# Kernel optimization log

Hardware: AMD Instinct MI355X
Metric: run time of the kernel (lower is better)

Reference implementation:

```python
import jax, jax.numpy as jnp
import numpy as np

N = 20000      # num clique nodes
E = 320000     # num edges
H = 256        # hidden_channels
OUT = 128      # out_channels
T = 3          # num_timesteps
NEG = 0.01     # GAT negative_slope
NA = 60000     # num atoms (unused arg sizing)


def setup_inputs() -> dict:
    key = jax.random.key(0)
    ks = jax.random.split(key, 12)
    s = 1.0 / np.sqrt(H)
    return {
        "x_clique": jax.random.normal(ks[0], (N, H), jnp.float32),
        "W_gat": jax.random.normal(ks[1], (H, H), jnp.float32) * s,
        "att_src": jax.random.normal(ks[2], (H,), jnp.float32) * s,
        "att_dst": jax.random.normal(ks[3], (H,), jnp.float32) * s,
        "gat_bias": jnp.zeros((H,), jnp.float32),
        "W_ih": jax.random.normal(ks[4], (3 * H, H), jnp.float32) * s,
        "W_hh": jax.random.normal(ks[5], (3 * H, H), jnp.float32) * s,
        "b_ih": jnp.zeros((3 * H,), jnp.float32),
        "b_hh": jnp.zeros((3 * H,), jnp.float32),
        "lin_W": jax.random.normal(ks[6], (OUT, H), jnp.float32) * s,
        "lin_b": jnp.zeros((OUT,), jnp.float32),
        "atom2clique_index": jax.random.randint(ks[7], (2, NA), 0, N, jnp.int64),
        "mol_batch": jax.random.randint(ks[8], (NA,), 0, 32, jnp.int64),
        "clique_batch": jax.random.randint(ks[9], (N,), 0, 32, jnp.int64),
        "clique_edge_index": jax.random.randint(ks[10], (2, E), 0, N, jnp.int64),
    }


def _gat_conv(h, W_gat, att_src, att_dst, gat_bias, src, dst):
    # PyG GATConv, heads=1, no self loops. h: [N,H]
    xp = h @ W_gat.T                                   # [N,H]
    a_e = jax.nn.leaky_relu((xp @ att_src)[src] + (xp @ att_dst)[dst], NEG)  # [E]
    # segment softmax over destination nodes
    m = jax.ops.segment_max(a_e, dst, num_segments=N)  # [N] (-inf for empty)
    e = jnp.exp(a_e - m[dst])                          # [E]
    denom = jax.ops.segment_sum(e, dst, num_segments=N)
    coef = e / jnp.maximum(denom[dst], 1e-16)          # [E]
    out = jax.ops.segment_sum(coef[:, None] * xp[src], dst, num_segments=N)
    return out + gat_bias


def _gru_cell(x, h, W_ih, W_hh, b_ih, b_hh):
    gx = x @ W_ih.T + b_ih                             # [N,3H]
    gh = h @ W_hh.T + b_hh                             # [N,3H]
    xr, xz, xn = jnp.split(gx, 3, axis=-1)
    hr, hz, hn = jnp.split(gh, 3, axis=-1)
    r = jax.nn.sigmoid(xr + hr)
    z = jax.nn.sigmoid(xz + hz)
    n = jnp.tanh(xn + r * hn)
    return (1.0 - z) * n + z * h


def reference(x_clique, W_gat, att_src, att_dst, gat_bias, W_ih, W_hh, b_ih, b_hh,
              lin_W, lin_b, atom2clique_index, mol_batch, clique_batch,
              clique_edge_index):
    src = clique_edge_index[0]
    dst = clique_edge_index[1]
    h = x_clique
    for _ in range(T):  # fixed, small timestep count
        m = _gat_conv(h, W_gat, att_src, att_dst, gat_bias, src, dst)
        m = jax.nn.elu(m)  # dropout p=0.0 -> identity
        h = _gru_cell(m, h, W_ih, W_hh, b_ih, b_hh)
    return h @ lin_W.T + lin_b  # [N, OUT]
```

## Files before the change

### kernel.cpp

```cpp
#include <hip/hip_runtime.h>
#include <math.h>

#define NNODES 20000
#define NROWP  20096
#define NEDGES 320000
#define HDIM   256
#define ODIM   128
#define TSTEPS 3
#define KCAT   512

typedef __bf16 bf16x8 __attribute__((ext_vector_type(8)));
typedef __bf16 bf16x4 __attribute__((ext_vector_type(4)));
typedef float  f32x4  __attribute__((ext_vector_type(4)));

#define LOG2E 1.44269504f
__device__ __forceinline__ float fexp2_(float x){ return __builtin_amdgcn_exp2f(x); }
__device__ __forceinline__ float frcp_(float x){ return __builtin_amdgcn_rcpf(x); }
__device__ __forceinline__ float fsig_(float x){ return frcp_(1.f + fexp2_(-LOG2E*x)); }
__device__ __forceinline__ float ftanh_(float x){ float t = fexp2_(2.f*LOG2E*x); return 1.f - 2.f*frcp_(t+1.f); }
__device__ __forceinline__ float felu_(float x){ return (x>0.f)? x : (fexp2_(LOG2E*x)-1.f); }

__device__ __forceinline__ void load_lds16(const void* g, void* l){
  __builtin_amdgcn_global_load_lds((const __attribute__((address_space(1))) void*)g,
                                   (__attribute__((address_space(3))) void*)l, 16, 0, 0);
}

__device__ __forceinline__ bf16x8 lds_frag64(const __bf16* Ls, int rowbase, int lane, int kk){
  int row = rowbase + (lane&15);
  int g = (lane>>4) + (kk<<2);
  int slot = (row<<3) + (g ^ (row&7));
  return *(const bf16x8*)&Ls[slot<<3];
}

template<int NWG>
__device__ __forceinline__ int xcd_swz(int b){
  constexpr int Q = NWG/8, R = NWG%8;
  int x = b & 7, i = b >> 3;
  if (R == 0) return x*Q + i;
  return (x < R) ? (x*(Q+1) + i) : (R*(Q+1) + (x-R)*Q + i);
}

#define WAIT_VM(n) asm volatile("s_waitcnt vmcnt(" #n ")" ::: "memory")
#define WAIT_LGKM0 asm volatile("s_waitcnt lgkmcnt(0)" ::: "memory")


__global__ void setup1_kernel(const int* __restrict__ dst, int* __restrict__ deg,
                              const float* __restrict__ xc, __bf16* __restrict__ Acat,
                              const float* __restrict__ Wih, const float* __restrict__ Whh,
                              const float* __restrict__ Wg, const float* __restrict__ Lw,
                              __bf16* __restrict__ Bf, __bf16* __restrict__ wgb,
                              __bf16* __restrict__ lwb, float* __restrict__ asad){
  int i = blockIdx.x*blockDim.x + threadIdx.x;
  if (i < NEDGES) atomicAdd(&deg[dst[i]], 1);
  if (i < NNODES*64){
    int row = i>>6, c = (i&63)<<2;
    float4 v = *(const float4*)&xc[(size_t)row*HDIM + c];
    bf16x4 o; o[0]=(__bf16)v.x; o[1]=(__bf16)v.y; o[2]=(__bf16)v.z; o[3]=(__bf16)v.w;
    *(bf16x4*)&Acat[(size_t)row*KCAT + 256 + c] = o;
  }
  if (i < 1024*128){
    int row = i>>7, kc = (i&127)<<2;
    int gate = row>>8, c = row&255;
    float4 v = make_float4(0,0,0,0);
    if (gate==0 || gate==1){
      v = (kc<256) ? *(const float4*)&Wih[(size_t)(gate*256+c)*HDIM + kc]
                   : *(const float4*)&Whh[(size_t)(gate*256+c)*HDIM + kc-256];
    } else if (gate==2){
      if (kc<256) v = *(const float4*)&Wih[(size_t)(512+c)*HDIM + kc];
    } else {
      if (kc>=256) v = *(const float4*)&Whh[(size_t)(512+c)*HDIM + kc-256];
    }
    bf16x4 o; o[0]=(__bf16)v.x; o[1]=(__bf16)v.y; o[2]=(__bf16)v.z; o[3]=(__bf16)v.w;
    *(bf16x4*)&Bf[(size_t)row*KCAT + kc] = o;
  } else if (i < 1024*128 + 256*64){
    int j = i - 1024*128;
    float4 v = ((const float4*)Wg)[j];
    bf16x4 o; o[0]=(__bf16)v.x; o[1]=(__bf16)v.y; o[2]=(__bf16)v.z; o[3]=(__bf16)v.w;
    ((bf16x4*)wgb)[j] = o;
  } else if (i < 1024*128 + 256*64 + 128*64){
    int j = i - 1024*128 - 256*64;
    float4 v = ((const float4*)Lw)[j];
    bf16x4 o; o[0]=(__bf16)v.x; o[1]=(__bf16)v.y; o[2]=(__bf16)v.z; o[3]=(__bf16)v.w;
    ((bf16x4*)lwb)[j] = o;
  }
  if (i < 2*NNODES) asad[i] = 0.f;
}

__global__ void scan_kernel(const int* __restrict__ deg, int* __restrict__ rowptr){
  const int PER = 20;
  int tid = threadIdx.x, lane = tid&63, w = tid>>6;
  int base = tid*PER;
  int v[PER]; int s = 0;
  #pragma unroll
  for (int k=0;k<PER;k++){
    v[k] = (base+k < NNODES)? deg[base+k] : 0;
    s += v[k];
  }
  int incl = s;
  #pragma unroll
  for (int off=1; off<64; off<<=1){
    int t = __shfl_up(incl, off);
    if (lane >= off) incl += t;
  }
  __shared__ int wtot[16];
  if (lane==63) wtot[w] = incl;
  __syncthreads();
  if (w==0 && lane<16){
    int x = wtot[lane];
    #pragma unroll
    for (int off=1; off<16; off<<=1){
      int t = __shfl_up(x, off);
      if (lane >= off) x += t;
    }
    wtot[lane] = x;
  }
  __syncthreads();
  int wbase = (w>0)? wtot[w-1] : 0;
  int run = wbase + incl - s;
  #pragma unroll
  for (int k=0;k<PER;k++){
    if (base+k < NNODES) rowptr[base+k] = run;
    run += v[k];
  }
  if (tid==1023) rowptr[NNODES] = wbase + incl;
}

__global__ void scatter_kernel(const int* __restrict__ src, const int* __restrict__ dst,
                               const int* __restrict__ rowptr, int* __restrict__ fill,
                               int* __restrict__ ssrc){
  int e = blockIdx.x*blockDim.x + threadIdx.x;
  if (e < NEDGES){
    int d = dst[e];
    int pos = rowptr[d] + atomicAdd(&fill[d], 1);
    ssrc[pos] = src[e];
  }
}

template<int YC, bool F32OUT, bool ALPHA, int NWG>
__global__ __launch_bounds__(256,3)
void mfma_gemm_sm(const __bf16* __restrict__ A, int lda,
                  const __bf16* __restrict__ B,
                  const float* __restrict__ bias,
                  __bf16* __restrict__ Cb, float* __restrict__ Cf,
                  int ldc, int Mreal,
                  const float* __restrict__ att_s, const float* __restrict__ att_d,
                  float* __restrict__ as_, float* __restrict__ ad_){
  __shared__ __bf16 As[2][64*64];
  __shared__ __bf16 Bs[2][128*64];
  int wgid = xcd_swz<NWG>(blockIdx.x);
  int r0 = (wgid/YC)*64, c0 = (wgid%YC)*128;
  int tx = threadIdx.x, lane = tx&63, w = tx>>6;
  int rbase = (w&1)*32, cbase = (w>>1)*64;
  f32x4 acc[2][4] = {};

  auto stage = [&](int k0, int s){
    #pragma unroll
    for (int q=0;q<2;q++){
      int idx = q*256 + w*64 + lane;
      int row = idx>>3, kg = (idx&7) ^ (row&7);
      load_lds16(A + (size_t)(r0+row)*lda + k0 + (kg<<3),
                 (char*)&As[s][0] + (q*256 + w*64)*16);
    }
    #pragma unroll
    for (int q=0;q<4;q++){
      int idx = q*256 + w*64 + lane;
      int row = idx>>3, kg = (idx&7) ^ (row&7);
      load_lds16(B + (size_t)(c0+row)*HDIM + k0 + (kg<<3),
                 (char*)&Bs[s][0] + (q*256 + w*64)*16);
    }
  };

  stage(0, 0);
  stage(64, 1);
  #pragma unroll
  for (int t=0; t<HDIM/64; t++){
    const int cur = t & 1;
    if (t == HDIM/64-1) { WAIT_VM(0); } else { WAIT_VM(6); }
    __builtin_amdgcn_s_barrier();
    #pragma unroll
    for (int kk=0;kk<2;kk++){
      bf16x8 a[2], bb[4];
      #pragma unroll
      for (int i=0;i<2;i++) a[i] = lds_frag64(&As[cur][0], rbase + i*16, lane, kk);
      #pragma unroll
      for (int j=0;j<4;j++) bb[j] = lds_frag64(&Bs[cur][0], cbase + j*16, lane, kk);
      #pragma unroll
      for (int i=0;i<2;i++)
        #pragma unroll
        for (int j=0;j<4;j++)
          acc[i][j] = __builtin_amdgcn_mfma_f32_16x16x32_bf16(a[i], bb[j], acc[i][j], 0,0,0);
    }
    WAIT_LGKM0;
    __builtin_amdgcn_s_barrier();
    if (t+2 < HDIM/64) stage((t+2)*64, cur);
  }
  int grb = r0 + rbase, gcb = c0 + cbase;
  #pragma unroll
  for (int i=0;i<2;i++){
    #pragma unroll
    for (int j=0;j<4;j++){
      int gc = gcb + j*16 + (lane&15);
      float bv = F32OUT ? bias[gc] : 0.f;
      #pragma unroll
      for (int r=0;r<4;r++){
        int gr = grb + i*16 + ((lane>>4)<<2) + r;
        if (gr >= Mreal) continue;
        float v = acc[i][j][r] + bv;
        if (F32OUT) Cf[(size_t)gr*ldc + gc] = v;
        else        Cb[(size_t)gr*ldc + gc] = (__bf16)v;
      }
    }
  }
  if (ALPHA){
    float ps[2][4] = {}, pd[2][4] = {};
    #pragma unroll
    for (int j=0;j<4;j++){
      int gc = gcb + j*16 + (lane&15);
      float sv = att_s[gc], dv = att_d[gc];
      #pragma unroll
      for (int i=0;i<2;i++)
        #pragma unroll
        for (int r=0;r<4;r++){
          ps[i][r] += acc[i][j][r]*sv;
          pd[i][r] += acc[i][j][r]*dv;
        }
    }
    #pragma unroll
    for (int m=1;m<16;m<<=1){
      #pragma unroll
      for (int i=0;i<2;i++)
        #pragma unroll
        for (int r=0;r<4;r++){
          ps[i][r] += __shfl_xor(ps[i][r], m);
          pd[i][r] += __shfl_xor(pd[i][r], m);
        }
    }
    if ((lane&15)==0){
      #pragma unroll
      for (int i=0;i<2;i++)
        #pragma unroll
        for (int r=0;r<4;r++){
          int gr = grb + i*16 + ((lane>>4)<<2) + r;
          if (gr < Mreal){
            atomicAdd(&as_[gr], ps[i][r]);
            atomicAdd(&ad_[gr], pd[i][r]);
          }
        }
    }
  }
}

__global__ __launch_bounds__(256,4)
void gat_aggregate_kernel(const __bf16* __restrict__ xpb, const float* __restrict__ as_,
                          const float* __restrict__ ad_, const int* __restrict__ rowptr,
                          const int* __restrict__ ssrc, const float* __restrict__ gat_bias,
                          __bf16* __restrict__ Acat){
  int node = blockIdx.x*4 + (threadIdx.x>>6);
  int lane = threadIdx.x & 63;
  if (node >= NNODES) return;
  int beg = rowptr[node], end = rowptr[node+1];
  int deg = end - beg;
  float adv = ad_[node];
  int half = lane>>5, col = lane&31;

  float acc[8] = {0,0,0,0,0,0,0,0};

  if (deg <= 64){
    float a = -INFINITY; int sreg = 0;
    if (lane < deg){
      sreg = ssrc[beg+lane];
      a = as_[sreg] + adv;
      a = (a>0.f)? a : 0.01f*a;
    }
    float mx = a;
    #pragma unroll
    for (int off=32; off; off>>=1) mx = fmaxf(mx, __shfl_xor(mx,off));
    float e = (lane<deg)? fexp2_(LOG2E*(a-mx)) : 0.f;
    float sm = e;
    #pragma unroll
    for (int off=32; off; off>>=1) sm += __shfl_xor(sm,off);
    float creg = e*frcp_(fmaxf(sm,1e-16f));

    int j = 0;
    for (; j+16<=deg; j+=16){
      float cc[8]; int rr[8]; bf16x8 vv[8];
      #pragma unroll
      for (int k=0;k<8;k++){
        cc[k] = __shfl(creg, j+2*k+half);
        rr[k] = __shfl(sreg, j+2*k+half);
      }
      #pragma unroll
      for (int k=0;k<8;k++) vv[k] = *(const bf16x8*)&xpb[(size_t)rr[k]*HDIM + col*8];
      #pragma unroll
      for (int k=0;k<8;k++)
        #pragma unroll
        for (int t=0;t<8;t++) acc[t] += cc[k]*(float)vv[k][t];
    }
    for (; j+8<=deg; j+=8){
      float cc[4]; int rr[4]; bf16x8 vv[4];
      #pragma unroll
      for (int k=0;k<4;k++){
        cc[k] = __shfl(creg, j+2*k+half);
        rr[k] = __shfl(sreg, j+2*k+half);
      }
      #pragma unroll
      for (int k=0;k<4;k++) vv[k] = *(const bf16x8*)&xpb[(size_t)rr[k]*HDIM + col*8];
      #pragma unroll
      for (int k=0;k<4;k++)
        #pragma unroll
        for (int t=0;t<8;t++) acc[t] += cc[k]*(float)vv[k][t];
    }
    for (; j+4<=deg; j+=4){
      float c0=__shfl(creg,j+half),  c1=__shfl(creg,j+2+half);
      int   r0=__shfl(sreg,j+half),  r1=__shfl(sreg,j+2+half);
      bf16x8 v0 = *(const bf16x8*)&xpb[(size_t)r0*HDIM + col*8];
      bf16x8 v1 = *(const bf16x8*)&xpb[(size_t)r1*HDIM + col*8];
      #pragma unroll
      for (int t=0;t<8;t++) acc[t] += c0*(float)v0[t] + c1*(float)v1[t];
    }
    for (; j<deg; j+=2){
      int jj = j + half;
      float cf = __shfl(creg, jj);
      int   rw = __shfl(sreg, jj);
      if (jj < deg){
        bf16x8 v = *(const bf16x8*)&xpb[(size_t)rw*HDIM + col*8];
        #pragma unroll
        for (int t=0;t<8;t++) acc[t] += cf*(float)v[t];
      }
    }
  } else {
    float mx = -INFINITY;
    for (int e=beg+lane; e<end; e+=64){
      float a = as_[ssrc[e]] + adv;
      a = (a>0.f)? a : 0.01f*a;
      mx = fmaxf(mx, a);
    }
    #pragma unroll
    for (int off=32; off; off>>=1) mx = fmaxf(mx, __shfl_xor(mx,off));
    float sm = 0.f;
    for (int e=beg+lane; e<end; e+=64){
      float a = as_[ssrc[e]] + adv;
      a = (a>0.f)? a : 0.01f*a;
      sm += fexp2_(LOG2E*(a-mx));
    }
    #pragma unroll
    for (int off=32; off; off>>=1) sm += __shfl_xor(sm,off);
    float rsc = frcp_(fmaxf(sm,1e-16f));
    for (int j=0; j<deg; j+=2){
      int jj = j + half;
      if (jj < deg){
        int rw = ssrc[beg+jj];
        float a = as_[rw] + adv;
        a = (a>0.f)? a : 0.01f*a;
        float cf = fexp2_(LOG2E*(a-mx))*rsc;
        bf16x8 v = *(const bf16x8*)&xpb[(size_t)rw*HDIM + col*8];
        #pragma unroll
        for (int t=0;t<8;t++) acc[t] += cf*(float)v[t];
      }
    }
  }

  #pragma unroll
  for (int t=0;t<8;t++) acc[t] += __shfl_down(acc[t], 32);
  if (half==0){
    float4 b0 = *(const float4*)&gat_bias[col*8];
    float4 b1 = *(const float4*)&gat_bias[col*8+4];
    float bb[8] = {b0.x,b0.y,b0.z,b0.w,b1.x,b1.y,b1.z,b1.w};
    bf16x8 ov;
    #pragma unroll
    for (int t=0;t<8;t++) ov[t] = (__bf16)felu_(acc[t]+bb[t]);
    *(bf16x8*)&Acat[(size_t)node*KCAT + col*8] = ov;
  }
}

#define RB128 (NROWP/128)
__global__ __launch_bounds__(256,4)
void gru_mfma_kernel(const __bf16* __restrict__ Acat, __bf16* __restrict__ AcatN,
                     const __bf16* __restrict__ Bf,
                     const float* __restrict__ bih, const float* __restrict__ bhh,
                     float* __restrict__ as_, float* __restrict__ ad_){
  __shared__ __bf16 As[128*64];
  __shared__ __bf16 Bs[96*64];
  int wgid = xcd_swz<RB128*8>(blockIdx.x);
  int r0 = (wgid>>3)*128, c0 = (wgid&7)*32;
  int tx = threadIdx.x, lane = tx&63, w = tx>>6;
  int rbase = w*32;
  f32x4 acc[4][2][2] = {};

  auto stage = [&](int k0, int tg){
    #pragma unroll
    for (int q=0;q<4;q++){
      int idx = q*256 + w*64 + lane;
      int row = idx>>3, kg = (idx&7) ^ (row&7);
      load_lds16(Acat + (size_t)(r0+row)*KCAT + k0 + (kg<<3),
                 (char*)As + (q*256 + w*64)*16);
    }
    #pragma unroll
    for (int q=0;q<3;q++){
      int idx = q*256 + w*64 + lane;
      int row = idx>>3, kg = (idx&7) ^ (row&7);
      int gsel = row>>5;
      int grow = (gsel==2 ? tg : gsel)*256 + c0 + (row&31);
      load_lds16(Bf + (size_t)grow*KCAT + k0 + (kg<<3),
                 (char*)Bs + (q*256 + w*64)*16);
    }
  };

  #pragma unroll
  for (int t=0; t<KCAT/64; t++){
    stage(t*64, (t<4)?2:3);
    __syncthreads();
    #pragma unroll
    for (int kk=0;kk<2;kk++){
      bf16x8 a[2], b0[2], b1[2], bt[2];
      #pragma unroll
      for (int i=0;i<2;i++) a[i] = lds_frag64(As, rbase + i*16, lane, kk);
      #pragma unroll
      for (int j=0;j<2;j++){
        b0[j] = lds_frag64(Bs, 0  + j*16, lane, kk);
        b1[j] = lds_frag64(Bs, 32 + j*16, lane, kk);
        bt[j] = lds_frag64(Bs, 64 + j*16, lane, kk);
      }
      #pragma unroll
      for (int i=0;i<2;i++)
        #pragma unroll
        for (int j=0;j<2;j++){
          acc[0][i][j] = __builtin_amdgcn_mfma_f32_16x16x32_bf16(a[i], b0[j], acc[0][i][j], 0,0,0);
          acc[1][i][j] = __builtin_amdgcn_mfma_f32_16x16x32_bf16(a[i], b1[j], acc[1][i][j], 0,0,0);
          if (t < 4)
            acc[2][i][j] = __builtin_amdgcn_mfma_f32_16x16x32_bf16(a[i], bt[j], acc[2][i][j], 0,0,0);
          else
            acc[3][i][j] = __builtin_amdgcn_mfma_f32_16x16x32_bf16(a[i], bt[j], acc[3][i][j], 0,0,0);
        }
    }
    __syncthreads();
  }
  int grb = r0 + rbase;
  #pragma unroll
  for (int i=0;i<2;i++){
    #pragma unroll
    for (int j=0;j<2;j++){
      int gc = c0 + j*16 + (lane&15);
      float br_ = bih[gc]     + bhh[gc];
      float bz_ = bih[256+gc] + bhh[256+gc];
      float bnx = bih[512+gc];
      float bnh = bhh[512+gc];
      #pragma unroll
      for (int r=0;r<4;r++){
        int gr = grb + i*16 + ((lane>>4)<<2) + r;
        if (gr >= NNODES) continue;
        float hold = (float)Acat[(size_t)gr*KCAT + 256 + gc];
        float rr = fsig_(acc[0][i][j][r] + br_);
        float zz = fsig_(acc[1][i][j][r] + bz_);
        float nn = ftanh_(acc[2][i][j][r] + bnx + rr*(acc[3][i][j][r] + bnh));
        AcatN[(size_t)gr*KCAT + 256 + gc] = (__bf16)((1.f-zz)*nn + zz*hold);
      }
    }
  }
  if ((wgid&7)==0 && (lane&15)==0){
    #pragma unroll
    for (int i=0;i<2;i++)
      #pragma unroll
      for (int r=0;r<4;r++){
        int gr = grb + i*16 + ((lane>>4)<<2) + r;
        if (gr < NNODES){ as_[gr] = 0.f; ad_[gr] = 0.f; }
      }
  }
}

extern "C" void kernel_launch(void* const* d_in, const int* in_sizes, int n_in,
                              void* d_out, int out_size, void* d_ws, size_t ws_size,
                              hipStream_t stream) {
  const float* x_clique = (const float*)d_in[0];
  const float* W_gat    = (const float*)d_in[1];
  const float* att_src  = (const float*)d_in[2];
  const float* att_dst  = (const float*)d_in[3];
  const float* gat_bias = (const float*)d_in[4];
  const float* W_ih     = (const float*)d_in[5];
  const float* W_hh     = (const float*)d_in[6];
  const float* b_ih     = (const float*)d_in[7];
  const float* b_hh     = (const float*)d_in[8];
  const float* lin_W    = (const float*)d_in[9];
  const float* lin_b    = (const float*)d_in[10];
  const int*   eidx     = (const int*)d_in[14];
  float* out = (float*)d_out;

  const int* src = eidx;
  const int* dst = eidx + NEDGES;

  const size_t ACAT = (size_t)NROWP*KCAT;
  __bf16* AcA  = (__bf16*)d_ws;
  __bf16* AcB  = AcA + ACAT;
  __bf16* xpb  = AcB + ACAT;
  __bf16* Bf   = xpb + (size_t)NROWP*HDIM;
  __bf16* wgb  = Bf  + (size_t)1024*KCAT;
  __bf16* lwb  = wgb + (size_t)HDIM*HDIM;
  float* as_   = (float*)(lwb + (size_t)ODIM*HDIM);
  float* ad_   = as_ + NNODES;
  int* deg     = (int*)(ad_ + NNODES);
  int* fill    = deg + NNODES;
  int* rowptr  = fill + NNODES;
  int* ssrc    = rowptr + (NNODES+1);

  hipMemsetAsync(deg, 0, 2*NNODES*sizeof(int), stream);
  setup1_kernel<<<NNODES*64/256, 256, 0, stream>>>(
      dst, deg, x_clique, AcA, W_ih, W_hh, W_gat, lin_W, Bf, wgb, lwb, as_);
  scan_kernel<<<1, 1024, 0, stream>>>(deg, rowptr);
  scatter_kernel<<<(NEDGES+255)/256, 256, 0, stream>>>(src, dst, rowptr, fill, ssrc);

  const int RB64 = NROWP/64;
  __bf16* Ac = AcA;
  __bf16* An = AcB;
  for (int t=0; t<TSTEPS; t++){
    mfma_gemm_sm<2,false,true,(NROWP/64)*2><<<RB64*2, 256, 0, stream>>>(
        Ac + 256, KCAT, wgb, nullptr, xpb, nullptr, HDIM, NNODES,
        att_src, att_dst, as_, ad_);
    gat_aggregate_kernel<<<(NNODES+3)/4, 256, 0, stream>>>(xpb, as_, ad_, rowptr, ssrc, gat_bias, Ac);
    gru_mfma_kernel<<<RB128*8, 256, 0, stream>>>(Ac, An, Bf, b_ih, b_hh, as_, ad_);
    __bf16* tmp = Ac; Ac = An; An = tmp;
  }
  mfma_gemm_sm<1,true,false,NROWP/64><<<RB64, 256, 0, stream>>>(
      Ac + 256, KCAT, lwb, lin_b, nullptr, out, ODIM, NNODES,
      nullptr, nullptr, nullptr, nullptr);
}
```

Before: 336.6 us.

## Fuse CSR build into setup and first GEMM launches, dropping memset/scan/scatter kernels

The degree histogram and prefix scan move into one extra 1024-thread block of the setup kernel, using packed 16-bit counters in LDS, so the memset and the separate scan kernel go away. The scatter of source indices becomes extra blocks appended to the first timestep's GAT projection GEMM launch. Those blocks use a copied rowptr as an atomic cursor, so the separate fill array is no longer needed. This cuts three launches and one memset. The cost is that a single block now serially processes all 320k edges for the histogram, which could sit on the critical path.

Measured after the change: 354.6 us. 1.05x slower.

```diff
diff --git a/kernel.cpp b/kernel.cpp
--- a/kernel.cpp
+++ b/kernel.cpp
@@ -8,6 +8,9 @@
 #define ODIM   128
 #define TSTEPS 3
 #define KCAT   512
+#define RB64   (NROWP/64)
+#define RB128  (NROWP/128)
+#define SCAT_NB ((NEDGES+255)/256)
 
 typedef __bf16 bf16x8 __attribute__((ext_vector_type(8)));
 typedef __bf16 bf16x4 __attribute__((ext_vector_type(4)));
@@ -44,14 +47,70 @@
 #define WAIT_LGKM0 asm volatile("s_waitcnt lgkmcnt(0)" ::: "memory")
 
 
-__global__ void setup1_kernel(const int* __restrict__ dst, int* __restrict__ deg,
-                              const float* __restrict__ xc, __bf16* __restrict__ Acat,
-                              const float* __restrict__ Wih, const float* __restrict__ Whh,
-                              const float* __restrict__ Wg, const float* __restrict__ Lw,
-                              __bf16* __restrict__ Bf, __bf16* __restrict__ wgb,
-                              __bf16* __restrict__ lwb, float* __restrict__ asad){
-  int i = blockIdx.x*blockDim.x + threadIdx.x;
-  if (i < NEDGES) atomicAdd(&deg[dst[i]], 1);
+__global__ __launch_bounds__(1024)
+void setup_fat(const int* __restrict__ src, const int* __restrict__ dst,
+               const float* __restrict__ xc, __bf16* __restrict__ Acat,
+               const float* __restrict__ Wih, const float* __restrict__ Whh,
+               const float* __restrict__ Wg, const float* __restrict__ Lw,
+               __bf16* __restrict__ Bf, __bf16* __restrict__ wgb,
+               __bf16* __restrict__ lwb, float* __restrict__ asad,
+               int* __restrict__ rowptr, int* __restrict__ rowptr2){
+  __shared__ int ldeg[NNODES/2];
+  __shared__ int wtot[16];
+  int tx = threadIdx.x;
+
+  if (blockIdx.x == 1250){
+    for (int k=tx; k<NNODES/2; k+=1024) ldeg[k] = 0;
+    __syncthreads();
+    for (int e=tx*4; e<NEDGES; e+=4096){
+      int4 d4 = *(const int4*)&dst[e];
+      atomicAdd(&ldeg[d4.x>>1], 1 << ((d4.x&1)<<4));
+      atomicAdd(&ldeg[d4.y>>1], 1 << ((d4.y&1)<<4));
+      atomicAdd(&ldeg[d4.z>>1], 1 << ((d4.z&1)<<4));
+      atomicAdd(&ldeg[d4.w>>1], 1 << ((d4.w&1)<<4));
+    }
+    __syncthreads();
+    const int PER = 20;
+    int lane = tx&63, w = tx>>6;
+    int base = tx*PER;
+    int v[PER]; int s = 0;
+    #pragma unroll
+    for (int k=0;k<PER;k++){
+      int n = base+k;
+      v[k] = (n < NNODES)? ((ldeg[n>>1] >> ((n&1)<<4)) & 0xffff) : 0;
+      s += v[k];
+    }
+    int incl = s;
+    #pragma unroll
+    for (int off=1; off<64; off<<=1){
+      int t = __shfl_up(incl, off);
+      if (lane >= off) incl += t;
+    }
+    if (lane==63) wtot[w] = incl;
+    __syncthreads();
+    if (w==0 && lane<16){
+      int x = wtot[lane];
+      #pragma unroll
+      for (int off=1; off<16; off<<=1){
+        int t = __shfl_up(x, off);
+        if (lane >= off) x += t;
+      }
+      wtot[lane] = x;
+    }
+    __syncthreads();
+    int wbase = (w>0)? wtot[w-1] : 0;
+    int run = wbase + incl - s;
+    #pragma unroll
+    for (int k=0;k<PER;k++){
+      int n = base+k;
+      if (n < NNODES){ rowptr[n] = run; rowptr2[n] = run; }
+      run += v[k];
+    }
+    if (tx==1023) rowptr[NNODES] = wbase + incl;
+    return;
+  }
+
+  int i = blockIdx.x*1024 + tx;
   if (i < NNODES*64){
     int row = i>>6, c = (i&63)<<2;
     float4 v = *(const float4*)&xc[(size_t)row*HDIM + c];
@@ -86,57 +145,7 @@
   if (i < 2*NNODES) asad[i] = 0.f;
 }
 
-__global__ void scan_kernel(const int* __restrict__ deg, int* __restrict__ rowptr){
-  const int PER = 20;
-  int tid = threadIdx.x, lane = tid&63, w = tid>>6;
-  int base = tid*PER;
-  int v[PER]; int s = 0;
-  #pragma unroll
-  for (int k=0;k<PER;k++){
-    v[k] = (base+k < NNODES)? deg[base+k] : 0;
-    s += v[k];
-  }
-  int incl = s;
-  #pragma unroll
-  for (int off=1; off<64; off<<=1){
-    int t = __shfl_up(incl, off);
-    if (lane >= off) incl += t;
-  }
-  __shared__ int wtot[16];
-  if (lane==63) wtot[w] = incl;
-  __syncthreads();
-  if (w==0 && lane<16){
-    int x = wtot[lane];
-    #pragma unroll
-    for (int off=1; off<16; off<<=1){
-      int t = __shfl_up(x, off);
-      if (lane >= off) x += t;
-    }
-    wtot[lane] = x;
-  }
-  __syncthreads();
-  int wbase = (w>0)? wtot[w-1] : 0;
-  int run = wbase + incl - s;
-  #pragma unroll
-  for (int k=0;k<PER;k++){
-    if (base+k < NNODES) rowptr[base+k] = run;
-    run += v[k];
-  }
-  if (tid==1023) rowptr[NNODES] = wbase + incl;
-}
-
-__global__ void scatter_kernel(const int* __restrict__ src, const int* __restrict__ dst,
-                               const int* __restrict__ rowptr, int* __restrict__ fill,
-                               int* __restrict__ ssrc){
-  int e = blockIdx.x*blockDim.x + threadIdx.x;
-  if (e < NEDGES){
-    int d = dst[e];
-    int pos = rowptr[d] + atomicAdd(&fill[d], 1);
-    ssrc[pos] = src[e];
-  }
-}
-
-template<int YC, bool F32OUT, bool ALPHA, int NWG>
+template<int YC, bool F32OUT, bool ALPHA, int NWG, bool SCAT>
 __global__ __launch_bounds__(256,3)
 void mfma_gemm_sm(const __bf16* __restrict__ A, int lda,
                   const __bf16* __restrict__ B,
@@ -144,7 +153,18 @@
                   __bf16* __restrict__ Cb, float* __restrict__ Cf,
                   int ldc, int Mreal,
                   const float* __restrict__ att_s, const float* __restrict__ att_d,
-                  float* __restrict__ as_, float* __restrict__ ad_){
+                  float* __restrict__ as_, float* __restrict__ ad_,
+                  const int* __restrict__ srcE, const int* __restrict__ dstE,
+                  int* __restrict__ rp2, int* __restrict__ ssrc){
+  if (SCAT && blockIdx.x >= NWG){
+    int e = (blockIdx.x - NWG)*256 + threadIdx.x;
+    if (e < NEDGES){
+      int d = dstE[e];
+      int pos = atomicAdd(&rp2[d], 1);
+      ssrc[pos] = srcE[e];
+    }
+    return;
+  }
   __shared__ __bf16 As[2][64*64];
   __shared__ __bf16 Bs[2][128*64];
   int wgid = xcd_swz<NWG>(blockIdx.x);
@@ -373,7 +393,6 @@
   }
 }
 
-#define RB128 (NROWP/128)
 __global__ __launch_bounds__(256,4)
 void gru_mfma_kernel(const __bf16* __restrict__ Acat, __bf16* __restrict__ AcatN,
                      const __bf16* __restrict__ Bf,
@@ -497,29 +516,31 @@
   __bf16* lwb  = wgb + (size_t)HDIM*HDIM;
   float* as_   = (float*)(lwb + (size_t)ODIM*HDIM);
   float* ad_   = as_ + NNODES;
-  int* deg     = (int*)(ad_ + NNODES);
-  int* fill    = deg + NNODES;
-  int* rowptr  = fill + NNODES;
-  int* ssrc    = rowptr + (NNODES+1);
-
-  hipMemsetAsync(deg, 0, 2*NNODES*sizeof(int), stream);
-  setup1_kernel<<<NNODES*64/256, 256, 0, stream>>>(
-      dst, deg, x_clique, AcA, W_ih, W_hh, W_gat, lin_W, Bf, wgb, lwb, as_);
-  scan_kernel<<<1, 1024, 0, stream>>>(deg, rowptr);
-  scatter_kernel<<<(NEDGES+255)/256, 256, 0, stream>>>(src, dst, rowptr, fill, ssrc);
-
-  const int RB64 = NROWP/64;
+  int* rowptr  = (int*)(ad_ + NNODES);
+  int* rowptr2 = rowptr + (NNODES+1);
+  int* ssrc    = rowptr2 + NNODES;
+
+  setup_fat<<<1251, 1024, 0, stream>>>(
+      src, dst, x_clique, AcA, W_ih, W_hh, W_gat, lin_W, Bf, wgb, lwb, as_,
+      rowptr, rowptr2);
+
   __bf16* Ac = AcA;
   __bf16* An = AcB;
   for (int t=0; t<TSTEPS; t++){
-    mfma_gemm_sm<2,false,true,(NROWP/64)*2><<<RB64*2, 256, 0, stream>>>(
-        Ac + 256, KCAT, wgb, nullptr, xpb, nullptr, HDIM, NNODES,
-        att_src, att_dst, as_, ad_);
+    if (t == 0){
+      mfma_gemm_sm<2,false,true,RB64*2,true><<<RB64*2 + SCAT_NB, 256, 0, stream>>>(
+          Ac + 256, KCAT, wgb, nullptr, xpb, nullptr, HDIM, NNODES,
+          att_src, att_dst, as_, ad_, src, dst, rowptr2, ssrc);
+    } else {
+      mfma_gemm_sm<2,false,true,RB64*2,false><<<RB64*2, 256, 0, stream>>>(
+          Ac + 256, KCAT, wgb, nullptr, xpb, nullptr, HDIM, NNODES,
+          att_src, att_dst, as_, ad_, nullptr, nullptr, nullptr, nullptr);
+    }
     gat_aggregate_kernel<<<(NNODES+3)/4, 256, 0, stream>>>(xpb, as_, ad_, rowptr, ssrc, gat_bias, Ac);
     gru_mfma_kernel<<<RB128*8, 256, 0, stream>>>(Ac, An, Bf, b_ih, b_hh, as_, ad_);
     __bf16* tmp = Ac; Ac = An; An = tmp;
   }
-  mfma_gemm_sm<1,true,false,NROWP/64><<<RB64, 256, 0, stream>>>(
+  mfma_gemm_sm<1,true,false,RB64,false><<<RB64, 256, 0, stream>>>(
       Ac + 256, KCAT, lwb, lin_b, nullptr, out, ODIM, NNODES,
-      nullptr, nullptr, nullptr, nullptr);
-}
+      nullptr, nullptr, nullptr, nullptr, nullptr, nullptr, nullptr, nullptr);
+}
```
